# Optimization experiments

Hardware: AMD Instinct MI355X
Metric: run time of the kernel (lower is better)

The kernel has to match this reference:

```python
import jax, jax.numpy as jnp
import numpy as np

N_NODES = 100000
N_EDGES = 1600000
IN_CH = 128
OUT_CH = 128

def setup_inputs() -> dict:
    key = jax.random.key(0)
    k1, k2, k3, k4, k5 = jax.random.split(key, 5)
    x = jax.random.normal(k1, (N_NODES, IN_CH), dtype=jnp.float32)
    src = jax.random.randint(k2, (N_EDGES,), 0, N_NODES, dtype=jnp.int64)
    dst = jax.random.randint(k3, (N_EDGES,), 0, N_NODES, dtype=jnp.int64)
    edge_index = jnp.stack([src, dst], axis=0)
    W = jax.random.normal(k4, (OUT_CH, IN_CH), dtype=jnp.float32) * (1.0 / np.sqrt(IN_CH))
    b = jax.random.normal(k5, (OUT_CH,), dtype=jnp.float32) * 0.01
    return {"x": x, "edge_index": edge_index, "W": W, "b": b}

def reference(x, edge_index, W, b):
    n = x.shape[0]
    src, dst = edge_index[0], edge_index[1]
    loop = jnp.arange(n, dtype=edge_index.dtype)
    src_all = jnp.concatenate([src, loop])  # [E+N]
    dst_all = jnp.concatenate([dst, loop])  # [E+N]
    # in-degree (with self loops) per node
    deg = jax.ops.segment_sum(jnp.ones_like(dst_all, dtype=x.dtype), dst_all, num_segments=n)
    norm = (deg[src_all] * deg[dst_all]) ** -0.5
    norm = jnp.where(jnp.isinf(norm), 0.0, norm)
    h = x @ W.T + b  # [N, out_ch]
    msg = h[src_all] * norm[:, None]  # [E+N, out_ch]
    out = jax.ops.segment_sum(msg, dst_all, num_segments=n)  # [N, out_ch]
    return out
```

## Files before the change

### kernel.cpp

```cpp
#include <hip/hip_runtime.h>
#include <hip/hip_bf16.h>


#define N_NODES 100000
#define N_EDGES 1600000
#define CH 128
#define NC 49
#define EPB 1024
#define NBLKA 1563
#define CAPB 48
#define BPU 23
#define NCHB 68
#define NFB 1563
#define FCAP 1280
#define STCAP 768

using bf16x8 = __attribute__((ext_vector_type(8))) short;
using f32x4  = __attribute__((ext_vector_type(4))) float;

__device__ inline unsigned short f2bf(float f) {
    unsigned u = __float_as_uint(f);
    u += 0x7fffu + ((u >> 16) & 1u);
    return (unsigned short)(u >> 16);
}
__device__ inline float bflo(unsigned u) { return __uint_as_float(u << 16); }
__device__ inline float bfhi(unsigned u) { return __uint_as_float(u & 0xffff0000u); }

__global__ __launch_bounds__(256) void k_place(const int* __restrict__ src,
                                               const int* __restrict__ dst,
                                               int* __restrict__ cntG,
                                               unsigned* __restrict__ E1,
                                               int* __restrict__ ftail) {
    __shared__ int hist[NC];
    __shared__ int boff[NC + 1];
    __shared__ int cur[NC];
    __shared__ unsigned stage[EPB];
    const int t    = threadIdx.x;
    const int bid  = blockIdx.x;
    const int base = bid * EPB;
    const int n    = min(EPB, N_EDGES - base);

    if (t < 2) { int i = bid * 2 + t; if (i < 1600) ftail[i] = 0; }
    if (t < NC) hist[t] = 0;
    __syncthreads();

    int s[4], d[4];
    {
        int idx = 4 * t;
        if (idx < n) {
            int4 sv = *(const int4*)&src[base + idx];
            int4 dv = *(const int4*)&dst[base + idx];
            s[0] = sv.x; s[1] = sv.y; s[2] = sv.z; s[3] = sv.w;
            d[0] = dv.x; d[1] = dv.y; d[2] = dv.z; d[3] = dv.w;
        } else {
            d[0] = d[1] = d[2] = d[3] = -1;
            s[0] = s[1] = s[2] = s[3] = 0;
        }
    }
#pragma unroll
    for (int j = 0; j < 4; ++j)
        if (d[j] >= 0) atomicAdd(&hist[d[j] >> 11], 1);
    __syncthreads();

    if (t < 64) {
        int v = (t < NC) ? hist[t] : 0;
#pragma unroll
        for (int off = 1; off < 64; off <<= 1) {
            int u = __shfl_up(v, off, 64);
            if (t >= off) v += u;
        }
        if (t < NC) boff[t + 1] = v;
        if (t == 0) boff[0] = 0;
    }
    __syncthreads();
    if (t < NC) cur[t] = boff[t];
    __syncthreads();

#pragma unroll
    for (int j = 0; j < 4; ++j)
        if (d[j] >= 0) {
            int k = d[j] >> 11;
            int pos = atomicAdd(&cur[k], 1);
            stage[pos] = ((unsigned)s[j] << 11) | (unsigned)(d[j] & 2047);
        }
    __syncthreads();

    if (t < NC) cntG[(size_t)t * NBLKA + bid] = min(hist[t], CAPB);

    const int tot = boff[NC];
    for (int i = t; i < tot; i += 256) {
        int lo = 0, hi = NC;
#pragma unroll
        for (int it = 0; it < 6; ++it) {
            int mid = (lo + hi) >> 1;
            bool c = (boff[mid] <= i);
            lo = c ? mid : lo;
            hi = c ? hi : mid;
        }
        int p = i - boff[lo];
        if (p < CAPB)
            E1[((size_t)lo * NBLKA + bid) * CAPB + p] = stage[i];
    }
}

__global__ __launch_bounds__(256) void k_sortB(const unsigned* __restrict__ E1,
                                               const int* __restrict__ cntG,
                                               int* __restrict__ ftail,
                                               unsigned* __restrict__ E2) {
    __shared__ int hist[32];
    __shared__ int boff[33];
    __shared__ int cur[32];
    __shared__ int gb[32];
    __shared__ int cnt[BPU];
    __shared__ unsigned stage[STCAP];
    const int cb  = blockIdx.x / NCHB;
    const int u   = blockIdx.x % NCHB;
    const int sb0 = u * BPU;
    const int t   = threadIdx.x;

    if (t < 32) hist[t] = 0;
    if (t < BPU) {
        int sb = sb0 + t;
        cnt[t] = (sb < NBLKA) ? cntG[(size_t)cb * NBLKA + sb] : 0;
    }
    __syncthreads();

    const unsigned* e1 = E1 + ((size_t)cb * NBLKA + sb0) * CAPB;

    for (int i = t; i < BPU * CAPB; i += 256) {
        int sb = i / CAPB, sl = i - sb * CAPB;
        if (sl < cnt[sb]) atomicAdd(&hist[(e1[i] >> 6) & 31], 1);
    }
    __syncthreads();

    if (t < 32) gb[t] = atomicAdd(&ftail[cb * 32 + t], hist[t]);
    if (t < 64) {
        int v = (t < 32) ? hist[t] : 0;
#pragma unroll
        for (int off = 1; off < 32; off <<= 1) {
            int w = __shfl_up(v, off, 64);
            if (t >= off) v += w;
        }
        if (t < 32) boff[t + 1] = v;
        if (t == 0) boff[0] = 0;
    }
    __syncthreads();
    if (t < 32) cur[t] = boff[t];
    __syncthreads();

    for (int i = t; i < BPU * CAPB; i += 256) {
        int sb = i / CAPB, sl = i - sb * CAPB;
        if (sl < cnt[sb]) {
            unsigned v = e1[i];
            int k = (v >> 6) & 31;
            int pos = atomicAdd(&cur[k], 1);
            if (pos < STCAP)
                stage[pos] = ((v >> 11) << 6) | (v & 63);
        }
    }
    __syncthreads();

    const int tot = min(boff[32], STCAP);
    for (int i = t; i < tot; i += 256) {
        int lo = 0, hi = 32;
#pragma unroll
        for (int it = 0; it < 5; ++it) {
            int mid = (lo + hi) >> 1;
            bool c = (boff[mid] <= i);
            lo = c ? mid : lo;
            hi = c ? hi : mid;
        }
        int p = gb[lo] + (i - boff[lo]);
        int fb = cb * 32 + lo;
        if (p < FCAP) E2[(size_t)fb * FCAP + p] = stage[i];
    }
}

__device__ inline void cvt8(const float4 a, const float4 b, bf16x8& h, bf16x8& l) {
    bf16x8 H, L;
#define CV(i, f) { unsigned short hb = f2bf(f); H[i] = (short)hb;               \
                   L[i] = (short)f2bf((f) - __uint_as_float((unsigned)hb << 16)); }
    CV(0, a.x) CV(1, a.y) CV(2, a.z) CV(3, a.w)
    CV(4, b.x) CV(5, b.y) CV(6, b.z) CV(7, b.w)
#undef CV
    h = H; l = L;
}

#define MFMA(a, b, c) __builtin_amdgcn_mfma_f32_16x16x32_bf16((a), (b), (c), 0, 0, 0)

__global__ __launch_bounds__(256) void k_gemm(const float* __restrict__ x,
                                              const float* __restrict__ W,
                                              const float* __restrict__ b,
                                              const unsigned* __restrict__ E2,
                                              const int* __restrict__ ftail,
                                              unsigned short* __restrict__ hs) {
    __shared__ __align__(16) unsigned short wh[CH * CH];
    __shared__ __align__(16) unsigned short wl[CH * CH];
    const int t = threadIdx.x;
    const int lane = t & 63;
    const int l15  = lane & 15;
    const int lhi  = lane >> 4;

    int* dbin = (int*)wh;
    if (t < 128) dbin[t] = 0;
    __syncthreads();
    {
        const int fb0 = blockIdx.x * 2;
        int n0 = ftail[fb0]; if (n0 > FCAP) n0 = FCAP;
        const unsigned* e0 = E2 + (size_t)fb0 * FCAP;
        for (int i = t; i < n0; i += 256) atomicAdd(&dbin[e0[i] & 63], 1);
        const int fb1 = fb0 + 1;
        if (fb1 < NFB) {
            int n1 = ftail[fb1]; if (n1 > FCAP) n1 = FCAP;
            const unsigned* e1p = E2 + (size_t)fb1 * FCAP;
            for (int i = t; i < n1; i += 256) atomicAdd(&dbin[64 + (e1p[i] & 63)], 1);
        }
    }
    __syncthreads();
    float rreg[2][4];
#pragma unroll
    for (int rf = 0; rf < 2; ++rf) {
        int lb = (t >> 6) * 32 + rf * 16 + lhi * 4;
#pragma unroll
        for (int j = 0; j < 4; ++j)
            rreg[rf][j] = rsqrtf((float)(dbin[lb + j] + 1));
    }
    __syncthreads();

    for (int c = t; c < 2048; c += 256) {
        int o   = c >> 4;
        int kk  = (c & 15) << 3;
        const float* wp = &W[(size_t)o * CH + kk];
        float4 w0 = *(const float4*)wp;
        float4 w1 = *(const float4*)(wp + 4);
        bf16x8 H, L;
        cvt8(w0, w1, H, L);
        unsigned boff = ((unsigned)((o << 8) | (kk << 1))) ^ ((unsigned)(o & 7) << 4);
        *(bf16x8*)((char*)wh + boff) = H;
        *(bf16x8*)((char*)wl + boff) = L;
    }
    __syncthreads();

    const int kc = lhi << 3;
    const int row_base = blockIdx.x * 128 + (t >> 6) * 32;

    int r0 = row_base + l15;       if (r0 > N_NODES - 1) r0 = N_NODES - 1;
    int r1 = row_base + 16 + l15;  if (r1 > N_NODES - 1) r1 = N_NODES - 1;
    const float* x0 = &x[(size_t)r0 * CH + kc];
    const float* x1 = &x[(size_t)r1 * CH + kc];

    float4 xa[4][2], xb[4][2];
#pragma unroll
    for (int ks = 0; ks < 4; ++ks) {
        xa[ks][0] = *(const float4*)(x0 + ks * 32);
        xa[ks][1] = *(const float4*)(x0 + ks * 32 + 4);
        xb[ks][0] = *(const float4*)(x1 + ks * 32);
        xb[ks][1] = *(const float4*)(x1 + ks * 32 + 4);
    }

    f32x4 acc[2][8];
#pragma unroll
    for (int rf = 0; rf < 2; ++rf)
#pragma unroll
        for (int cf = 0; cf < 8; ++cf)
            acc[rf][cf] = (f32x4){0.f, 0.f, 0.f, 0.f};

#pragma unroll
    for (int ks = 0; ks < 4; ++ks) {
        bf16x8 ah0, al0, ah1, al1;
        cvt8(xa[ks][0], xa[ks][1], ah0, al0);
        cvt8(xb[ks][0], xb[ks][1], ah1, al1);
        const unsigned kb = (unsigned)((ks * 32 + kc) << 1);
#pragma unroll
        for (int cf = 0; cf < 8; ++cf) {
            int o = cf * 16 + l15;
            unsigned boff = (((unsigned)(o << 8)) + kb) ^ ((unsigned)(o & 7) << 4);
            bf16x8 bh = *(const bf16x8*)((const char*)wh + boff);
            bf16x8 bl = *(const bf16x8*)((const char*)wl + boff);
            acc[0][cf] = MFMA(ah0, bh, acc[0][cf]);
            acc[1][cf] = MFMA(ah1, bh, acc[1][cf]);
            acc[0][cf] = MFMA(al0, bh, acc[0][cf]);
            acc[1][cf] = MFMA(al1, bh, acc[1][cf]);
            acc[0][cf] = MFMA(ah0, bl, acc[0][cf]);
            acc[1][cf] = MFMA(ah1, bl, acc[1][cf]);
        }
    }

    float bcol[8];
#pragma unroll
    for (int cf = 0; cf < 8; ++cf) bcol[cf] = b[cf * 16 + l15];

#pragma unroll
    for (int rf = 0; rf < 2; ++rf) {
        int rb = row_base + rf * 16 + lhi * 4;
        if (rb >= N_NODES) continue;
#pragma unroll
        for (int j = 0; j < 4; ++j) {
            size_t ro = (size_t)(rb + j) * CH;
            float ri = rreg[rf][j];
#pragma unroll
            for (int cf = 0; cf < 8; ++cf)
                hs[ro + cf * 16 + l15] = f2bf(ri * (acc[rf][cf][j] + bcol[cf]));
        }
    }
}

#define ACC8(u)                                                            \
    do {                                                                   \
        acc[0] += bflo((u).x); acc[1] += bfhi((u).x);                      \
        acc[2] += bflo((u).y); acc[3] += bfhi((u).y);                      \
        acc[4] += bflo((u).z); acc[5] += bfhi((u).z);                      \
        acc[6] += bflo((u).w); acc[7] += bfhi((u).w);                      \
    } while (0)

__global__ __launch_bounds__(256) void k_spmm(const unsigned* __restrict__ E2,
                                              const int* __restrict__ ftail,
                                              const unsigned short* __restrict__ hs,
                                              float* __restrict__ out,
                                              int fb0) {
    __shared__ int bins[64];
    __shared__ int boff[65];
    __shared__ int cur[64];
    __shared__ int srt[FCAP];
    const int fb    = blockIdx.x + fb0;
    const int node0 = fb * 64;
    const int t     = threadIdx.x;
    const unsigned* e2 = E2 + (size_t)fb * FCAP;
    const uint4* hp = (const uint4*)hs;

    if (t < 64) bins[t] = 0;
    int n = ftail[fb]; if (n > FCAP) n = FCAP;
    __syncthreads();

    for (int i = t; i < n; i += 256) atomicAdd(&bins[e2[i] & 63], 1);
    __syncthreads();

    if (t == 0) {
        int run = 0;
        for (int k = 0; k < 64; ++k) { boff[k] = run; run += bins[k]; }
        boff[64] = run;
    }
    __syncthreads();
    if (t < 64) cur[t] = boff[t];
    __syncthreads();

    for (int i = t; i < n; i += 256) {
        unsigned v = e2[i];
        int pos = atomicAdd(&cur[v & 63], 1);
        srt[pos] = (int)(v >> 6);
    }
    __syncthreads();

    const int grp  = t >> 4;
    const int lane = t & 15;
#pragma unroll
    for (int r = 0; r < 4; ++r) {
        const int nl   = grp * 4 + r;
        const int node = node0 + nl;
        if (node >= N_NODES) continue;
        float acc[8] = {};
        {
            uint4 u = hp[(size_t)node * 16 + lane];
            ACC8(u);
        }
        int e  = boff[nl];
        int e1 = boff[nl + 1];
        for (; e + 8 <= e1; e += 8) {
            int s0 = srt[e + 0], s1 = srt[e + 1], s2 = srt[e + 2], s3 = srt[e + 3];
            int s4 = srt[e + 4], s5 = srt[e + 5], s6 = srt[e + 6], s7 = srt[e + 7];
            uint4 u0 = hp[(size_t)s0 * 16 + lane];
            uint4 u1 = hp[(size_t)s1 * 16 + lane];
            uint4 u2 = hp[(size_t)s2 * 16 + lane];
            uint4 u3 = hp[(size_t)s3 * 16 + lane];
            uint4 u4 = hp[(size_t)s4 * 16 + lane];
            uint4 u5 = hp[(size_t)s5 * 16 + lane];
            uint4 u6 = hp[(size_t)s6 * 16 + lane];
            uint4 u7 = hp[(size_t)s7 * 16 + lane];
            ACC8(u0); ACC8(u1); ACC8(u2); ACC8(u3);
            ACC8(u4); ACC8(u5); ACC8(u6); ACC8(u7);
        }
        for (; e + 4 <= e1; e += 4) {
            int s0 = srt[e + 0];
            int s1 = srt[e + 1];
            int s2 = srt[e + 2];
            int s3 = srt[e + 3];
            uint4 u0 = hp[(size_t)s0 * 16 + lane];
            uint4 u1 = hp[(size_t)s1 * 16 + lane];
            uint4 u2 = hp[(size_t)s2 * 16 + lane];
            uint4 u3 = hp[(size_t)s3 * 16 + lane];
            ACC8(u0); ACC8(u1); ACC8(u2); ACC8(u3);
        }
        for (; e < e1; ++e) {
            uint4 u = hp[(size_t)srt[e] * 16 + lane];
            ACC8(u);
        }
        float ri = rsqrtf((float)(bins[nl] + 1));
        f32x4 o0, o1;
        o0[0] = ri * acc[0]; o0[1] = ri * acc[1]; o0[2] = ri * acc[2]; o0[3] = ri * acc[3];
        o1[0] = ri * acc[4]; o1[1] = ri * acc[5]; o1[2] = ri * acc[6]; o1[3] = ri * acc[7];
        *(f32x4*)&out[(size_t)node * CH + lane * 8]     = o0;
        *(f32x4*)&out[(size_t)node * CH + lane * 8 + 4] = o1;
    }
}

extern "C" void kernel_launch(void* const* d_in, const int* in_sizes, int n_in,
                              void* d_out, int out_size, void* d_ws, size_t ws_size,
                              hipStream_t stream) {
    const float* x  = (const float*)d_in[0];
    const int*   ei = (const int*)d_in[1];
    const float* W  = (const float*)d_in[2];
    const float* b  = (const float*)d_in[3];
    float* out = (float*)d_out;

    const int* src = (const int*)ei;
    const int* dst = (const int*)ei + N_EDGES;

    int*      ftail = (int*)d_ws;
    int*      cntG  = ftail + 1600;
    unsigned* E2    = (unsigned*)(cntG + 76608);
    unsigned short* hs = (unsigned short*)(E2 + (size_t)NFB * FCAP);
    unsigned* E1    = (unsigned*)hs;

    k_place<<<NBLKA, 256, 0, stream>>>(src, dst, cntG, E1, ftail);
    k_sortB<<<NC * NCHB, 256, 0, stream>>>(E1, cntG, ftail, E2);
    k_gemm<<<(N_NODES + 127) / 128, 256, 0, stream>>>(x, W, b, E2, ftail, hs);
    k_spmm<<<782, 256, 0, stream>>>(E2, ftail, hs, out, 0);
    k_spmm<<<NFB - 782, 256, 0, stream>>>(E2, ftail, hs, out, 782);
}
```

Baseline: 222.1 us.

## Precompute split-bf16 W in k_place and read it from global in GEMM

The hi/lo bf16 split of W now happens once, inside the first 64 blocks of k_place, and is written to a swizzled global buffer. k_gemm no longer builds a 64KB LDS copy of W per block and reads its B operands straight from global/L2. The GEMM also moves to 64 rows per block (one 16-row fragment per wave) with a grid of NFB blocks, which drops LDS use and register pressure so more blocks can be resident. The cost is that B fragments now come from global memory on every access and the grid doubles, and the W conversion adds a little work to k_place.

```diff
diff --git a/kernel.cpp b/kernel.cpp
--- a/kernel.cpp
+++ b/kernel.cpp
@@ -28,6 +28,9 @@
 
 __global__ __launch_bounds__(256) void k_place(const int* __restrict__ src,
                                                const int* __restrict__ dst,
+                                               const float* __restrict__ W,
+                                               unsigned short* __restrict__ whg,
+                                               unsigned short* __restrict__ wlg,
                                                int* __restrict__ cntG,
                                                unsigned* __restrict__ E1,
                                                int* __restrict__ ftail) {
@@ -41,6 +44,18 @@
     const int n    = min(EPB, N_EDGES - base);
 
     if (t < 2) { int i = bid * 2 + t; if (i < 1600) ftail[i] = 0; }
+
+    if (bid < 64) {
+        int idx = bid * 256 + t;
+        int o = idx >> 7, kk = idx & 127;
+        float v = W[idx];
+        unsigned short hb = f2bf(v);
+        unsigned short lb = f2bf(v - __uint_as_float((unsigned)hb << 16));
+        unsigned bo = ((unsigned)((o << 8) | (kk << 1))) ^ ((unsigned)(o & 7) << 4);
+        *(unsigned short*)((char*)whg + bo) = hb;
+        *(unsigned short*)((char*)wlg + bo) = lb;
+    }
+
     if (t < NC) hist[t] = 0;
     __syncthreads();
 
@@ -176,113 +191,78 @@
     }
 }
 
-__device__ inline void cvt8(const float4 a, const float4 b, bf16x8& h, bf16x8& l) {
-    bf16x8 H, L;
-#define CV(i, f) { unsigned short hb = f2bf(f); H[i] = (short)hb;               \
-                   L[i] = (short)f2bf((f) - __uint_as_float((unsigned)hb << 16)); }
-    CV(0, a.x) CV(1, a.y) CV(2, a.z) CV(3, a.w)
-    CV(4, b.x) CV(5, b.y) CV(6, b.z) CV(7, b.w)
-#undef CV
-    h = H; l = L;
-}
-
 #define MFMA(a, b, c) __builtin_amdgcn_mfma_f32_16x16x32_bf16((a), (b), (c), 0, 0, 0)
 
 __global__ __launch_bounds__(256) void k_gemm(const float* __restrict__ x,
-                                              const float* __restrict__ W,
+                                              const unsigned short* __restrict__ whg,
+                                              const unsigned short* __restrict__ wlg,
                                               const float* __restrict__ b,
                                               const unsigned* __restrict__ E2,
                                               const int* __restrict__ ftail,
                                               unsigned short* __restrict__ hs) {
-    __shared__ __align__(16) unsigned short wh[CH * CH];
-    __shared__ __align__(16) unsigned short wl[CH * CH];
-    const int t = threadIdx.x;
+    __shared__ int dbin[64];
+    const int t    = threadIdx.x;
     const int lane = t & 63;
     const int l15  = lane & 15;
     const int lhi  = lane >> 4;
-
-    int* dbin = (int*)wh;
-    if (t < 128) dbin[t] = 0;
+    const int wid  = t >> 6;
+    const int fb   = blockIdx.x;
+
+    if (t < 64) dbin[t] = 0;
     __syncthreads();
     {
-        const int fb0 = blockIdx.x * 2;
-        int n0 = ftail[fb0]; if (n0 > FCAP) n0 = FCAP;
-        const unsigned* e0 = E2 + (size_t)fb0 * FCAP;
+        int n0 = ftail[fb]; if (n0 > FCAP) n0 = FCAP;
+        const unsigned* e0 = E2 + (size_t)fb * FCAP;
         for (int i = t; i < n0; i += 256) atomicAdd(&dbin[e0[i] & 63], 1);
-        const int fb1 = fb0 + 1;
-        if (fb1 < NFB) {
-            int n1 = ftail[fb1]; if (n1 > FCAP) n1 = FCAP;
-            const unsigned* e1p = E2 + (size_t)fb1 * FCAP;
-            for (int i = t; i < n1; i += 256) atomicAdd(&dbin[64 + (e1p[i] & 63)], 1);
-        }
-    }
-    __syncthreads();
-    float rreg[2][4];
-#pragma unroll
-    for (int rf = 0; rf < 2; ++rf) {
-        int lb = (t >> 6) * 32 + rf * 16 + lhi * 4;
+    }
+    __syncthreads();
+    float rreg[4];
+    {
+        int lb = wid * 16 + lhi * 4;
 #pragma unroll
         for (int j = 0; j < 4; ++j)
-            rreg[rf][j] = rsqrtf((float)(dbin[lb + j] + 1));
-    }
-    __syncthreads();
-
-    for (int c = t; c < 2048; c += 256) {
-        int o   = c >> 4;
-        int kk  = (c & 15) << 3;
-        const float* wp = &W[(size_t)o * CH + kk];
-        float4 w0 = *(const float4*)wp;
-        float4 w1 = *(const float4*)(wp + 4);
-        bf16x8 H, L;
-        cvt8(w0, w1, H, L);
-        unsigned boff = ((unsigned)((o << 8) | (kk << 1))) ^ ((unsigned)(o & 7) << 4);
-        *(bf16x8*)((char*)wh + boff) = H;
-        *(bf16x8*)((char*)wl + boff) = L;
-    }
-    __syncthreads();
+            rreg[j] = rsqrtf((float)(dbin[lb + j] + 1));
+    }
 
     const int kc = lhi << 3;
-    const int row_base = blockIdx.x * 128 + (t >> 6) * 32;
-
-    int r0 = row_base + l15;       if (r0 > N_NODES - 1) r0 = N_NODES - 1;
-    int r1 = row_base + 16 + l15;  if (r1 > N_NODES - 1) r1 = N_NODES - 1;
+    const int row_base = fb * 64 + wid * 16;
+    int r0 = row_base + l15; if (r0 > N_NODES - 1) r0 = N_NODES - 1;
     const float* x0 = &x[(size_t)r0 * CH + kc];
-    const float* x1 = &x[(size_t)r1 * CH + kc];
-
-    float4 xa[4][2], xb[4][2];
+
+    float4 xa[4][2];
 #pragma unroll
     for (int ks = 0; ks < 4; ++ks) {
         xa[ks][0] = *(const float4*)(x0 + ks * 32);
         xa[ks][1] = *(const float4*)(x0 + ks * 32 + 4);
-        xb[ks][0] = *(const float4*)(x1 + ks * 32);
-        xb[ks][1] = *(const float4*)(x1 + ks * 32 + 4);
-    }
-
-    f32x4 acc[2][8];
-#pragma unroll
-    for (int rf = 0; rf < 2; ++rf)
-#pragma unroll
-        for (int cf = 0; cf < 8; ++cf)
-            acc[rf][cf] = (f32x4){0.f, 0.f, 0.f, 0.f};
+    }
+
+    f32x4 acc[8];
+#pragma unroll
+    for (int cf = 0; cf < 8; ++cf) acc[cf] = (f32x4){0.f, 0.f, 0.f, 0.f};
 
 #pragma unroll
     for (int ks = 0; ks < 4; ++ks) {
-        bf16x8 ah0, al0, ah1, al1;
-        cvt8(xa[ks][0], xa[ks][1], ah0, al0);
-        cvt8(xb[ks][0], xb[ks][1], ah1, al1);
+        bf16x8 ah, al;
+        {
+            float4 a = xa[ks][0], c = xa[ks][1];
+            bf16x8 H, L;
+#define CV(i, f) { unsigned short hb = f2bf(f); H[i] = (short)hb;               \
+                   L[i] = (short)f2bf((f) - __uint_as_float((unsigned)hb << 16)); }
+            CV(0, a.x) CV(1, a.y) CV(2, a.z) CV(3, a.w)
+            CV(4, c.x) CV(5, c.y) CV(6, c.z) CV(7, c.w)
+#undef CV
+            ah = H; al = L;
+        }
         const unsigned kb = (unsigned)((ks * 32 + kc) << 1);
 #pragma unroll
         for (int cf = 0; cf < 8; ++cf) {
             int o = cf * 16 + l15;
-            unsigned boff = (((unsigned)(o << 8)) + kb) ^ ((unsigned)(o & 7) << 4);
-            bf16x8 bh = *(const bf16x8*)((const char*)wh + boff);
-            bf16x8 bl = *(const bf16x8*)((const char*)wl + boff);
-            acc[0][cf] = MFMA(ah0, bh, acc[0][cf]);
-            acc[1][cf] = MFMA(ah1, bh, acc[1][cf]);
-            acc[0][cf] = MFMA(al0, bh, acc[0][cf]);
-            acc[1][cf] = MFMA(al1, bh, acc[1][cf]);
-            acc[0][cf] = MFMA(ah0, bl, acc[0][cf]);
-            acc[1][cf] = MFMA(ah1, bl, acc[1][cf]);
+            unsigned bo = (((unsigned)(o << 8)) + kb) ^ ((unsigned)(o & 7) << 4);
+            bf16x8 bh = *(const bf16x8*)((const char*)whg + bo);
+            bf16x8 bl = *(const bf16x8*)((const char*)wlg + bo);
+            acc[cf] = MFMA(ah, bh, acc[cf]);
+            acc[cf] = MFMA(al, bh, acc[cf]);
+            acc[cf] = MFMA(ah, bl, acc[cf]);
         }
     }
 
@@ -290,17 +270,15 @@
 #pragma unroll
     for (int cf = 0; cf < 8; ++cf) bcol[cf] = b[cf * 16 + l15];
 
-#pragma unroll
-    for (int rf = 0; rf < 2; ++rf) {
-        int rb = row_base + rf * 16 + lhi * 4;
-        if (rb >= N_NODES) continue;
+    int rb = row_base + lhi * 4;
+    if (rb < N_NODES) {
 #pragma unroll
         for (int j = 0; j < 4; ++j) {
             size_t ro = (size_t)(rb + j) * CH;
-            float ri = rreg[rf][j];
+            float ri = rreg[j];
 #pragma unroll
             for (int cf = 0; cf < 8; ++cf)
-                hs[ro + cf * 16 + l15] = f2bf(ri * (acc[rf][cf][j] + bcol[cf]));
+                hs[ro + cf * 16 + l15] = f2bf(ri * (acc[cf][j] + bcol[cf]));
         }
     }
 }
@@ -417,13 +395,15 @@
 
     int*      ftail = (int*)d_ws;
     int*      cntG  = ftail + 1600;
-    unsigned* E2    = (unsigned*)(cntG + 76608);
+    unsigned short* whg = (unsigned short*)(cntG + 76608);
+    unsigned short* wlg = whg + 16384;
+    unsigned* E2    = (unsigned*)(wlg + 16384);
     unsigned short* hs = (unsigned short*)(E2 + (size_t)NFB * FCAP);
     unsigned* E1    = (unsigned*)hs;
 
-    k_place<<<NBLKA, 256, 0, stream>>>(src, dst, cntG, E1, ftail);
+    k_place<<<NBLKA, 256, 0, stream>>>(src, dst, W, whg, wlg, cntG, E1, ftail);
     k_sortB<<<NC * NCHB, 256, 0, stream>>>(E1, cntG, ftail, E2);
-    k_gemm<<<(N_NODES + 127) / 128, 256, 0, stream>>>(x, W, b, E2, ftail, hs);
+    k_gemm<<<NFB, 256, 0, stream>>>(x, whg, wlg, b, E2, ftail, hs);
     k_spmm<<<782, 256, 0, stream>>>(E2, ftail, hs, out, 0);
     k_spmm<<<NFB - 782, 256, 0, stream>>>(E2, ftail, hs, out, 782);
 }
```

New measurement: 233.9 us. +5.3%, slower.

## Precompute split-bf16 W in place kernel and halve GEMM output columns per block

Applied to the files above, without the earlier changes.

The fp32-to-bf16 hi/lo split of W moves out of every GEMM block into the first 64 blocks of k_place, which write it to workspace. The GEMM block now copies a pre-swizzled 64-column slice of it into LDS, so LDS drops from 64KB to about 32KB. The grid doubles to 1564 blocks, each computing 64 output columns. x loads are software-pipelined one k-step ahead to cut register pressure and raise occupancy. The cost is that each row tile of x is read twice, the degree histogram is rebuilt by both blocks of a pair, and k_place does extra work.

```diff
diff --git a/kernel.cpp b/kernel.cpp
--- a/kernel.cpp
+++ b/kernel.cpp
@@ -28,6 +28,9 @@
 
 __global__ __launch_bounds__(256) void k_place(const int* __restrict__ src,
                                                const int* __restrict__ dst,
+                                               const float* __restrict__ W,
+                                               unsigned short* __restrict__ whg,
+                                               unsigned short* __restrict__ wlg,
                                                int* __restrict__ cntG,
                                                unsigned* __restrict__ E1,
                                                int* __restrict__ ftail) {
@@ -41,6 +44,18 @@
     const int n    = min(EPB, N_EDGES - base);
 
     if (t < 2) { int i = bid * 2 + t; if (i < 1600) ftail[i] = 0; }
+
+    if (bid < 64) {
+        int idx = bid * 256 + t;
+        int o = idx >> 7, kk = idx & 127;
+        float v = W[idx];
+        unsigned short hb = f2bf(v);
+        unsigned short lb = f2bf(v - __uint_as_float((unsigned)hb << 16));
+        unsigned bo = ((unsigned)((o << 8) | (kk << 1))) ^ ((unsigned)(o & 7) << 4);
+        *(unsigned short*)((char*)whg + bo) = hb;
+        *(unsigned short*)((char*)wlg + bo) = lb;
+    }
+
     if (t < NC) hist[t] = 0;
     __syncthreads();
 
@@ -176,36 +191,41 @@
     }
 }
 
-__device__ inline void cvt8(const float4 a, const float4 b, bf16x8& h, bf16x8& l) {
-    bf16x8 H, L;
-#define CV(i, f) { unsigned short hb = f2bf(f); H[i] = (short)hb;               \
-                   L[i] = (short)f2bf((f) - __uint_as_float((unsigned)hb << 16)); }
-    CV(0, a.x) CV(1, a.y) CV(2, a.z) CV(3, a.w)
-    CV(4, b.x) CV(5, b.y) CV(6, b.z) CV(7, b.w)
-#undef CV
-    h = H; l = L;
-}
-
 #define MFMA(a, b, c) __builtin_amdgcn_mfma_f32_16x16x32_bf16((a), (b), (c), 0, 0, 0)
 
 __global__ __launch_bounds__(256) void k_gemm(const float* __restrict__ x,
-                                              const float* __restrict__ W,
+                                              const unsigned short* __restrict__ whg,
+                                              const unsigned short* __restrict__ wlg,
                                               const float* __restrict__ b,
                                               const unsigned* __restrict__ E2,
                                               const int* __restrict__ ftail,
                                               unsigned short* __restrict__ hs) {
-    __shared__ __align__(16) unsigned short wh[CH * CH];
-    __shared__ __align__(16) unsigned short wl[CH * CH];
-    const int t = threadIdx.x;
+    __shared__ __align__(16) unsigned short lwh[64 * CH];
+    __shared__ __align__(16) unsigned short lwl[64 * CH];
+    __shared__ int dbin[128];
+    const int t    = threadIdx.x;
     const int lane = t & 63;
     const int l15  = lane & 15;
     const int lhi  = lane >> 4;
-
-    int* dbin = (int*)wh;
+    const int wid  = t >> 6;
+    const int rb_blk = blockIdx.x >> 1;
+    const int c0     = (blockIdx.x & 1) << 6;
+
+    {
+        const uint4* wh4 = (const uint4*)whg + c0 * 16;
+        const uint4* wl4 = (const uint4*)wlg + c0 * 16;
+        uint4* lh4 = (uint4*)lwh;
+        uint4* ll4 = (uint4*)lwl;
+        for (int i = t; i < 1024; i += 256) {
+            lh4[i] = wh4[i];
+            ll4[i] = wl4[i];
+        }
+    }
+
     if (t < 128) dbin[t] = 0;
     __syncthreads();
     {
-        const int fb0 = blockIdx.x * 2;
+        const int fb0 = rb_blk * 2;
         int n0 = ftail[fb0]; if (n0 > FCAP) n0 = FCAP;
         const unsigned* e0 = E2 + (size_t)fb0 * FCAP;
         for (int i = t; i < n0; i += 256) atomicAdd(&dbin[e0[i] & 63], 1);
@@ -220,63 +240,60 @@
     float rreg[2][4];
 #pragma unroll
     for (int rf = 0; rf < 2; ++rf) {
-        int lb = (t >> 6) * 32 + rf * 16 + lhi * 4;
+        int lb = wid * 32 + rf * 16 + lhi * 4;
 #pragma unroll
         for (int j = 0; j < 4; ++j)
             rreg[rf][j] = rsqrtf((float)(dbin[lb + j] + 1));
     }
-    __syncthreads();
-
-    for (int c = t; c < 2048; c += 256) {
-        int o   = c >> 4;
-        int kk  = (c & 15) << 3;
-        const float* wp = &W[(size_t)o * CH + kk];
-        float4 w0 = *(const float4*)wp;
-        float4 w1 = *(const float4*)(wp + 4);
-        bf16x8 H, L;
-        cvt8(w0, w1, H, L);
-        unsigned boff = ((unsigned)((o << 8) | (kk << 1))) ^ ((unsigned)(o & 7) << 4);
-        *(bf16x8*)((char*)wh + boff) = H;
-        *(bf16x8*)((char*)wl + boff) = L;
-    }
-    __syncthreads();
 
     const int kc = lhi << 3;
-    const int row_base = blockIdx.x * 128 + (t >> 6) * 32;
-
+    const int row_base = rb_blk * 128 + wid * 32;
     int r0 = row_base + l15;       if (r0 > N_NODES - 1) r0 = N_NODES - 1;
     int r1 = row_base + 16 + l15;  if (r1 > N_NODES - 1) r1 = N_NODES - 1;
     const float* x0 = &x[(size_t)r0 * CH + kc];
     const float* x1 = &x[(size_t)r1 * CH + kc];
 
-    float4 xa[4][2], xb[4][2];
+    f32x4 acc[2][4];
+#pragma unroll
+    for (int rf = 0; rf < 2; ++rf)
+#pragma unroll
+        for (int cf = 0; cf < 4; ++cf)
+            acc[rf][cf] = (f32x4){0.f, 0.f, 0.f, 0.f};
+
+    float4 ca0 = *(const float4*)(x0);
+    float4 ca1 = *(const float4*)(x0 + 4);
+    float4 cb0 = *(const float4*)(x1);
+    float4 cb1 = *(const float4*)(x1 + 4);
+
 #pragma unroll
     for (int ks = 0; ks < 4; ++ks) {
-        xa[ks][0] = *(const float4*)(x0 + ks * 32);
-        xa[ks][1] = *(const float4*)(x0 + ks * 32 + 4);
-        xb[ks][0] = *(const float4*)(x1 + ks * 32);
-        xb[ks][1] = *(const float4*)(x1 + ks * 32 + 4);
-    }
-
-    f32x4 acc[2][8];
-#pragma unroll
-    for (int rf = 0; rf < 2; ++rf)
-#pragma unroll
-        for (int cf = 0; cf < 8; ++cf)
-            acc[rf][cf] = (f32x4){0.f, 0.f, 0.f, 0.f};
-
-#pragma unroll
-    for (int ks = 0; ks < 4; ++ks) {
+        float4 na0, na1, nb0, nb1;
+        if (ks < 3) {
+            na0 = *(const float4*)(x0 + (ks + 1) * 32);
+            na1 = *(const float4*)(x0 + (ks + 1) * 32 + 4);
+            nb0 = *(const float4*)(x1 + (ks + 1) * 32);
+            nb1 = *(const float4*)(x1 + (ks + 1) * 32 + 4);
+        }
         bf16x8 ah0, al0, ah1, al1;
-        cvt8(xa[ks][0], xa[ks][1], ah0, al0);
-        cvt8(xb[ks][0], xb[ks][1], ah1, al1);
+        {
+            bf16x8 H, L;
+#define CV(i, f) { unsigned short hb = f2bf(f); H[i] = (short)hb;               \
+                   L[i] = (short)f2bf((f) - __uint_as_float((unsigned)hb << 16)); }
+            CV(0, ca0.x) CV(1, ca0.y) CV(2, ca0.z) CV(3, ca0.w)
+            CV(4, ca1.x) CV(5, ca1.y) CV(6, ca1.z) CV(7, ca1.w)
+            ah0 = H; al0 = L;
+            CV(0, cb0.x) CV(1, cb0.y) CV(2, cb0.z) CV(3, cb0.w)
+            CV(4, cb1.x) CV(5, cb1.y) CV(6, cb1.z) CV(7, cb1.w)
+            ah1 = H; al1 = L;
+#undef CV
+        }
         const unsigned kb = (unsigned)((ks * 32 + kc) << 1);
 #pragma unroll
-        for (int cf = 0; cf < 8; ++cf) {
-            int o = cf * 16 + l15;
-            unsigned boff = (((unsigned)(o << 8)) + kb) ^ ((unsigned)(o & 7) << 4);
-            bf16x8 bh = *(const bf16x8*)((const char*)wh + boff);
-            bf16x8 bl = *(const bf16x8*)((const char*)wl + boff);
+        for (int cf = 0; cf < 4; ++cf) {
+            int ol = cf * 16 + l15;
+            unsigned bo = (((unsigned)(ol << 8)) + kb) ^ ((unsigned)(ol & 7) << 4);
+            bf16x8 bh = *(const bf16x8*)((const char*)lwh + bo);
+            bf16x8 bl = *(const bf16x8*)((const char*)lwl + bo);
             acc[0][cf] = MFMA(ah0, bh, acc[0][cf]);
             acc[1][cf] = MFMA(ah1, bh, acc[1][cf]);
             acc[0][cf] = MFMA(al0, bh, acc[0][cf]);
@@ -284,11 +301,12 @@
             acc[0][cf] = MFMA(ah0, bl, acc[0][cf]);
             acc[1][cf] = MFMA(ah1, bl, acc[1][cf]);
         }
-    }
-
-    float bcol[8];
-#pragma unroll
-    for (int cf = 0; cf < 8; ++cf) bcol[cf] = b[cf * 16 + l15];
+        if (ks < 3) { ca0 = na0; ca1 = na1; cb0 = nb0; cb1 = nb1; }
+    }
+
+    float bcol[4];
+#pragma unroll
+    for (int cf = 0; cf < 4; ++cf) bcol[cf] = b[c0 + cf * 16 + l15];
 
 #pragma unroll
     for (int rf = 0; rf < 2; ++rf) {
@@ -296,10 +314,10 @@
         if (rb >= N_NODES) continue;
 #pragma unroll
         for (int j = 0; j < 4; ++j) {
-            size_t ro = (size_t)(rb + j) * CH;
+            size_t ro = (size_t)(rb + j) * CH + c0;
             float ri = rreg[rf][j];
 #pragma unroll
-            for (int cf = 0; cf < 8; ++cf)
+            for (int cf = 0; cf < 4; ++cf)
                 hs[ro + cf * 16 + l15] = f2bf(ri * (acc[rf][cf][j] + bcol[cf]));
         }
     }
@@ -417,13 +435,15 @@
 
     int*      ftail = (int*)d_ws;
     int*      cntG  = ftail + 1600;
-    unsigned* E2    = (unsigned*)(cntG + 76608);
+    unsigned short* whg = (unsigned short*)(cntG + 76608);
+    unsigned short* wlg = whg + 16384;
+    unsigned* E2    = (unsigned*)(wlg + 16384);
     unsigned short* hs = (unsigned short*)(E2 + (size_t)NFB * FCAP);
     unsigned* E1    = (unsigned*)hs;
 
-    k_place<<<NBLKA, 256, 0, stream>>>(src, dst, cntG, E1, ftail);
+    k_place<<<NBLKA, 256, 0, stream>>>(src, dst, W, whg, wlg, cntG, E1, ftail);
     k_sortB<<<NC * NCHB, 256, 0, stream>>>(E1, cntG, ftail, E2);
-    k_gemm<<<(N_NODES + 127) / 128, 256, 0, stream>>>(x, W, b, E2, ftail, hs);
+    k_gemm<<<1564, 256, 0, stream>>>(x, whg, wlg, b, E2, ftail, hs);
     k_spmm<<<782, 256, 0, stream>>>(E2, ftail, hs, out, 0);
     k_spmm<<<NFB - 782, 256, 0, stream>>>(E2, ftail, hs, out, 782);
 }
```

New measurement: 218.1 us. About the same (-1.8%).
